# Kernel tuning notes

Measured on AMD Instinct MI355X. Metric: run time of the kernel, lower is better.

## Reference

```python
import jax, jax.numpy as jnp
import numpy as np

B, HH, WW, C = 2, 128, 128, 256
HEADS, KA, DR = 8, 3, 4
D = C // DR // HEADS          # 8 per-head channels
KK = KA * KA                  # 9 neighborhood positions
ATTN_DIM = KK * HEADS         # 72
DIMS = (ATTN_DIM // 4, ATTN_DIM // 2, ATTN_DIM)  # gnConv dims [18,36,72] (order=3)
SD = sum(DIMS)                # 126
S = 1.0                       # self.scale = s in __init__ (overrides qk scale)


def conv2d(x, w, b, pad, groups=1):
    out = jax.lax.conv_general_dilated(
        x, w, (1, 1), [(pad, pad), (pad, pad)],
        dimension_numbers=("NCHW", "OIHW", "NCHW"), feature_group_count=groups)
    return out + b[None, :, None, None]


def setup_inputs() -> dict:
    key = jax.random.key(0)
    ks = jax.random.split(key, 16)
    def rn(i, shape, s=0.02):
        return jax.random.normal(ks[i], shape, dtype=jnp.float32) * s
    return {
        "x": jax.random.normal(ks[0], (B, HH * WW, C), dtype=jnp.float32),
        "qkv_w": rn(1, (C, 3 * C // DR)),
        "qkv_b": jnp.zeros((3 * C // DR,), jnp.float32),
        "dc1_dw_w": rn(2, (D, 1, KA, KA)),
        "dc1_dw_b": jnp.zeros((D,), jnp.float32),
        "dc1_pw_w": rn(3, (KK * D, D, 3, 3)),
        "dc1_pw_b": jnp.zeros((KK * D,), jnp.float32),
        "dc2_dw_w": rn(4, (D, 1, KA, KA)),
        "dc2_dw_b": jnp.zeros((D,), jnp.float32),
        "dc2_pw_w": rn(5, (KK * D, D, 3, 3)),
        "dc2_pw_b": jnp.zeros((KK * D,), jnp.float32),
        "rpb": rn(6, (1, HEADS, 1, KK, 1, 1)),
        "pin_w": rn(7, (2 * ATTN_DIM, ATTN_DIM, 1, 1)),
        "pin_b": jnp.zeros((2 * ATTN_DIM,), jnp.float32),
        "dw7_w": rn(8, (SD, 1, 7, 7)),
        "dw7_b": jnp.zeros((SD,), jnp.float32),
        "dw5_w": rn(9, (SD, 1, 5, 5)),
        "dw5_b": jnp.zeros((SD,), jnp.float32),
        "dw3_w": rn(10, (SD, 1, 3, 3)),
        "dw3_b": jnp.zeros((SD,), jnp.float32),
        "pw1_w": rn(11, (DIMS[1], DIMS[0], 1, 1)),
        "pw1_b": jnp.zeros((DIMS[1],), jnp.float32),
        "pw2_w": rn(12, (DIMS[2], DIMS[1], 1, 1)),
        "pw2_b": jnp.zeros((DIMS[2],), jnp.float32),
        "pout_w": rn(13, (ATTN_DIM, ATTN_DIM, 1, 1)),
        "pout_b": jnp.zeros((ATTN_DIM,), jnp.float32),
        "proj_w": rn(14, (C // DR, C)),
        "proj_b": jnp.zeros((C,), jnp.float32),
        "H": HH,
        "W": WW,
    }


def reference(x, qkv_w, qkv_b, dc1_dw_w, dc1_dw_b, dc1_pw_w, dc1_pw_b,
              dc2_dw_w, dc2_dw_b, dc2_pw_w, dc2_pw_b, rpb, pin_w, pin_b,
              dw7_w, dw7_b, dw5_w, dw5_b, dw3_w, dw3_b,
              pw1_w, pw1_b, pw2_w, pw2_b, pout_w, pout_b, proj_w, proj_b, H, W):
    Bx, N, Cx = x.shape
    xi = x.reshape(Bx, H, W, Cx)
    qkv = xi @ qkv_w + qkv_b                                   # (B,H,W,3C/DR)
    f = jnp.transpose(qkv, (0, 3, 1, 2)).reshape(Bx * HEADS, 3 * D, H, W)
    q = (f[:, :D] * S).reshape(Bx, HEADS, D, 1, H, W)
    k_in = f[:, D:2 * D]                                       # (B*heads, D, H, W)
    v_in = f[:, 2 * D:]

    def dep(y):  # shared dep_conv + dep_conv1: KAxKA depthwise then 3x3 D->KK*D expand
        a = conv2d(conv2d(y, dc1_dw_w, dc1_dw_b, KA // 2, groups=D), dc1_pw_w, dc1_pw_b, 1)
        b2 = conv2d(conv2d(y, dc2_dw_w, dc2_dw_b, KA // 2, groups=D), dc2_pw_w, dc2_pw_b, 1)
        return (a + b2).reshape(Bx, HEADS, D, KK, H, W)

    k = dep(k_in) + rpb                                        # relative position bias
    v = dep(v_in)
    attn1 = jax.nn.softmax((q * k).sum(2, keepdims=True), axis=3)  # (B,heads,1,KK,H,W)

    # gnConv (recursive gated conv) on attention maps
    attn = attn1.reshape(Bx, HEADS * KK, H, W)                 # (B,72,H,W)
    fused = conv2d(attn, pin_w, pin_b, 0)                      # (B,144,H,W)
    pwa, abc = fused[:, :DIMS[0]], fused[:, DIMS[0]:]          # 18 / 126
    dw = conv2d(abc, dw7_w, dw7_b, 3, groups=SD)
    dw = conv2d(jax.nn.relu(dw), dw5_w, dw5_b, 2, groups=SD)
    dw = conv2d(jax.nn.relu(dw), dw3_w, dw3_b, 1, groups=SD) * S
    d0 = dw[:, :DIMS[0]]
    d1 = dw[:, DIMS[0]:DIMS[0] + DIMS[1]]
    d2 = dw[:, DIMS[0] + DIMS[1]:]
    g = pwa * d0
    g = conv2d(g, pw1_w, pw1_b, 0) * d1
    g = conv2d(g, pw2_w, pw2_b, 0) * d2
    g = conv2d(g, pout_w, pout_b, 0).reshape(Bx, HEADS, 1, KK, H, W)

    out = ((g * v) + (attn1 * v)).sum(3).reshape(Bx, Cx // DR, H, W)
    out = jnp.transpose(out, (0, 2, 3, 1)) @ proj_w + proj_b   # Linear C/DR -> C
    return out.reshape(Bx, N, Cx)
```

## Files before the change

kernel.cpp:

```cpp
#include <hip/hip_runtime.h>

#define IH 128
#define IW 128
#define NPI (IH*IW)

__global__ __launch_bounds__(256) void k_wt(const float* __restrict__ w1,
                                            const float* __restrict__ w2,
                                            const float* __restrict__ pin_w,
                                            const float* __restrict__ pw1_w,
                                            const float* __restrict__ pw2_w,
                                            const float* __restrict__ pout_w,
                                            float* __restrict__ wT,
                                            float* __restrict__ pinT,
                                            float* __restrict__ pw1T,
                                            float* __restrict__ pw2T,
                                            float* __restrict__ poutT) {
  int i = blockIdx.x * 256 + threadIdx.x;
  if (i < 5184) {
    int c = i / 72, dkk = i % 72;
    wT[dkk * 144 + c]      = w1[i];
    wT[dkk * 144 + 72 + c] = w2[i];
  } else if (i < 5184 + 10368) {
    int f = i - 5184;
    pinT[(f % 72) * 144 + f / 72] = pin_w[f];
  } else if (i < 5184 + 10368 + 648) {
    int f = i - 5184 - 10368;
    pw1T[(f % 18) * 36 + f / 18] = pw1_w[f];
  } else if (i < 5184 + 10368 + 648 + 2592) {
    int f = i - 5184 - 10368 - 648;
    pw2T[(f % 36) * 72 + f / 36] = pw2_w[f];
  } else if (i < 5184 + 10368 + 648 + 2592 + 5184) {
    int f = i - 5184 - 10368 - 648 - 2592;
    poutT[(f % 72) * 72 + f / 72] = pout_w[f];
  }
}

__global__ __launch_bounds__(256) void k_qkv(const float* __restrict__ x,
                                             const float* __restrict__ w,
                                             const float* __restrict__ bias,
                                             float* __restrict__ f) {
  __shared__ float xs[16][68];
  __shared__ float ws[16][196];
  int t = threadIdx.x;
  int p0 = blockIdx.x * 64;
  int b = p0 >> 14;
  int pp = p0 & (NPI - 1);
  int tx = t & 15, ty = t >> 4;
  int pxb = tx * 4;
  int jb = ty * 12;
  float acc[48];
#pragma unroll
  for (int jj = 0; jj < 12; ++jj) {
    float bv = bias[jb + jj];
#pragma unroll
    for (int px = 0; px < 4; ++px) acc[jj * 4 + px] = bv;
  }
  int spx = t >> 2;
  int sk = (t & 3) * 4;
#pragma unroll 1
  for (int c0 = 0; c0 < 256; c0 += 16) {
    float4 xv = *reinterpret_cast<const float4*>(x + (size_t)(p0 + spx) * 256 + c0 + sk);
    xs[sk + 0][spx] = xv.x;
    xs[sk + 1][spx] = xv.y;
    xs[sk + 2][spx] = xv.z;
    xs[sk + 3][spx] = xv.w;
#pragma unroll
    for (int r = 0; r < 3; ++r) {
      int flat = (r * 256 + t) * 4;
      int kk = flat / 192, jj = flat % 192;
      float4 wv = *reinterpret_cast<const float4*>(w + (size_t)(c0 + kk) * 192 + jj);
      *reinterpret_cast<float4*>(&ws[kk][jj]) = wv;
    }
    __syncthreads();
#pragma unroll 4
    for (int k = 0; k < 16; ++k) {
      float4 xr = *reinterpret_cast<const float4*>(&xs[k][pxb]);
      float4 w0 = *reinterpret_cast<const float4*>(&ws[k][jb]);
      float4 w1 = *reinterpret_cast<const float4*>(&ws[k][jb + 4]);
      float4 w2 = *reinterpret_cast<const float4*>(&ws[k][jb + 8]);
      const float xv4[4] = {xr.x, xr.y, xr.z, xr.w};
      const float wv12[12] = {w0.x, w0.y, w0.z, w0.w, w1.x, w1.y, w1.z, w1.w,
                              w2.x, w2.y, w2.z, w2.w};
#pragma unroll
      for (int jj = 0; jj < 12; ++jj)
#pragma unroll
        for (int px = 0; px < 4; ++px)
          acc[jj * 4 + px] = __builtin_fmaf(wv12[jj], xv4[px], acc[jj * 4 + px]);
    }
    __syncthreads();
  }
#pragma unroll
  for (int jj = 0; jj < 12; ++jj) {
    float4 o;
    o.x = acc[jj * 4 + 0]; o.y = acc[jj * 4 + 1];
    o.z = acc[jj * 4 + 2]; o.w = acc[jj * 4 + 3];
    *reinterpret_cast<float4*>(
        &f[((size_t)(b * 192 + jb + jj)) * NPI + pp + pxb]) = o;
  }
}

template <int MODE>
__global__ __launch_bounds__(256, 1) void k_dep(const float* __restrict__ f,
    const float* __restrict__ dwW1, const float* __restrict__ dwB1,
    const float* __restrict__ dwW2, const float* __restrict__ dwB2,
    const float* __restrict__ wT,  const float* __restrict__ pwB1,
    const float* __restrict__ pwB2, const float* __restrict__ rpb,
    const float* __restrict__ gout, const float* __restrict__ attn_in,
    float* __restrict__ outp) {
  __shared__ float kin[8][20][20];
  __shared__ float dwa[8][18][20];
  __shared__ float dwb[8][18][20];
  int t = threadIdx.x;
  int tile = blockIdx.x;
  int bh = blockIdx.y;
  int h = bh & 7;
  int y0 = (tile >> 3) << 4, x0 = (tile & 7) << 4;
  const float* src = f + ((size_t)(bh * 24 + (MODE ? 16 : 8))) * NPI;
  for (int idx = t; idx < 8 * 20 * 20; idx += 256) {
    int c = idx / 400, r = idx % 400, yy = r / 20, xx = r % 20;
    int ay = y0 - 2 + yy, ax = x0 - 2 + xx;
    float v = 0.f;
    if ((unsigned)ay < (unsigned)IH && (unsigned)ax < (unsigned)IW)
      v = src[c * NPI + ay * IW + ax];
    kin[c][yy][xx] = v;
  }
  __syncthreads();
  for (int idx = t; idx < 8 * 18 * 18; idx += 256) {
    int c = idx / 324, r = idx % 324, yy = r / 18, xx = r % 18;
    int ay = y0 - 1 + yy, ax = x0 - 1 + xx;
    float va = 0.f, vb = 0.f;
    if ((unsigned)ay < (unsigned)IH && (unsigned)ax < (unsigned)IW) {
      va = dwB1[c]; vb = dwB2[c];
#pragma unroll
      for (int ky = 0; ky < 3; ++ky)
#pragma unroll
        for (int kx = 0; kx < 3; ++kx) {
          float s = kin[c][yy + ky][xx + kx];
          va = __builtin_fmaf(dwW1[c * 9 + ky * 3 + kx], s, va);
          vb = __builtin_fmaf(dwW2[c * 9 + ky * 3 + kx], s, vb);
        }
    }
    dwa[c][yy][xx] = va;
    dwb[c][yy][xx] = vb;
  }
  __syncthreads();
  int ly = t >> 4, lx = t & 15;
  int p = (y0 + ly) * IW + (x0 + lx);
  float acc[72];
#pragma unroll
  for (int c = 0; c < 72; ++c) {
    acc[c] = pwB1[c] + pwB2[c];
    if (MODE == 0) acc[c] += rpb[h * 9 + (c % 9)];
  }
#pragma unroll 1
  for (int d = 0; d < 8; ++d) {
#pragma unroll
    for (int t9 = 0; t9 < 9; ++t9) {
      const int ky = t9 / 3, kx = t9 % 3;
      const float v1 = dwa[d][ly + ky][lx + kx];
      const float v2 = dwb[d][ly + ky][lx + kx];
      const float* wp = wT + (size_t)(d * 9 + t9) * 144;
#pragma unroll
      for (int c = 0; c < 72; ++c) {
        acc[c] = __builtin_fmaf(wp[c], v1, acc[c]);
        acc[c] = __builtin_fmaf(wp[72 + c], v2, acc[c]);
      }
    }
  }
  if (MODE == 0) {
    float q[8];
#pragma unroll
    for (int d = 0; d < 8; ++d) q[d] = f[((size_t)(bh * 24 + d)) * NPI + p];
    float e[9];
    float m = -1e30f;
#pragma unroll
    for (int kk = 0; kk < 9; ++kk) {
      float s = 0.f;
#pragma unroll
      for (int d = 0; d < 8; ++d) s = __builtin_fmaf(q[d], acc[d * 9 + kk], s);
      e[kk] = s;
      m = fmaxf(m, s);
    }
    float sum = 0.f;
#pragma unroll
    for (int kk = 0; kk < 9; ++kk) { e[kk] = __expf(e[kk] - m); sum += e[kk]; }
    float r = 1.f / sum;
#pragma unroll
    for (int kk = 0; kk < 9; ++kk)
      outp[((size_t)(bh * 9 + kk)) * NPI + p] = e[kk] * r;
  } else {
    float coef[9];
#pragma unroll
    for (int kk = 0; kk < 9; ++kk)
      coef[kk] = gout[((size_t)(bh * 9 + kk)) * NPI + p] +
                 attn_in[((size_t)(bh * 9 + kk)) * NPI + p];
#pragma unroll
    for (int d = 0; d < 8; ++d) {
      float s = 0.f;
#pragma unroll
      for (int kk = 0; kk < 9; ++kk) s = __builtin_fmaf(coef[kk], acc[d * 9 + kk], s);
      outp[((size_t)(bh * 8 + d)) * NPI + p] = s;
    }
  }
}

__global__ __launch_bounds__(256, 2) void k_pin(const float* __restrict__ attn,
                                                const float* __restrict__ pinT,
                                                const float* __restrict__ bias,
                                                float* __restrict__ fused) {
  int t = threadIdx.x, lane = t & 63;
  int wv = t >> 6;
  int gp = blockIdx.x * 64 + lane;
  int b = gp >> 14, p = gp & (NPI - 1);
  const float* ap = attn + (size_t)b * 72 * NPI + p;
  int jbase = wv * 36;
  float acc[36];
#pragma unroll
  for (int jj = 0; jj < 36; ++jj) acc[jj] = bias[jbase + jj];
#pragma unroll 2
  for (int i = 0; i < 72; ++i) {
    float ai = ap[(size_t)i * NPI];
    const float* wp = pinT + i * 144 + jbase;
#pragma unroll
    for (int jj = 0; jj < 36; ++jj)
      acc[jj] = __builtin_fmaf(wp[jj], ai, acc[jj]);
  }
#pragma unroll
  for (int jj = 0; jj < 36; ++jj)
    fused[((size_t)b * 144 + jbase + jj) * NPI + p] = acc[jj];
}

__global__ __launch_bounds__(256) void k_dwchain(const float* __restrict__ fused,
    const float* __restrict__ w7, const float* __restrict__ b7,
    const float* __restrict__ w5, const float* __restrict__ b5,
    const float* __restrict__ w3, const float* __restrict__ b3,
    float* __restrict__ dwout) {
  __shared__ float s_in[44][44];
  __shared__ float s_t7[38][38];
  __shared__ float s_t5[34][34];
  int t = threadIdx.x;
  int tile = blockIdx.x;
  int c = blockIdx.y;
  int b = blockIdx.z;
  int y0 = (tile >> 2) << 5, x0 = (tile & 3) << 5;
  const float* src = fused + ((size_t)b * 144 + 18 + c) * NPI;
  for (int idx = t; idx < 44 * 44; idx += 256) {
    int yy = idx / 44, xx = idx % 44;
    int ay = y0 - 6 + yy, ax = x0 - 6 + xx;
    s_in[yy][xx] = ((unsigned)ay < (unsigned)IH && (unsigned)ax < (unsigned)IW)
                       ? src[ay * IW + ax] : 0.f;
  }
  __syncthreads();
  for (int idx = t; idx < 38 * 38; idx += 256) {
    int yy = idx / 38, xx = idx % 38;
    int ay = y0 - 3 + yy, ax = x0 - 3 + xx;
    float s = 0.f;
    if ((unsigned)ay < (unsigned)IH && (unsigned)ax < (unsigned)IW) {
      s = b7[c];
#pragma unroll
      for (int ky = 0; ky < 7; ++ky)
#pragma unroll
        for (int kx = 0; kx < 7; ++kx)
          s = __builtin_fmaf(w7[c * 49 + ky * 7 + kx], s_in[yy + ky][xx + kx], s);
      s = fmaxf(s, 0.f);
    }
    s_t7[yy][xx] = s;
  }
  __syncthreads();
  for (int idx = t; idx < 34 * 34; idx += 256) {
    int yy = idx / 34, xx = idx % 34;
    int ay = y0 - 1 + yy, ax = x0 - 1 + xx;
    float s = 0.f;
    if ((unsigned)ay < (unsigned)IH && (unsigned)ax < (unsigned)IW) {
      s = b5[c];
#pragma unroll
      for (int ky = 0; ky < 5; ++ky)
#pragma unroll
        for (int kx = 0; kx < 5; ++kx)
          s = __builtin_fmaf(w5[c * 25 + ky * 5 + kx], s_t7[yy + ky][xx + kx], s);
      s = fmaxf(s, 0.f);
    }
    s_t5[yy][xx] = s;
  }
  __syncthreads();
  for (int idx = t; idx < 32 * 32; idx += 256) {
    int py = idx >> 5, px = idx & 31;
    float s = b3[c];
#pragma unroll
    for (int ky = 0; ky < 3; ++ky)
#pragma unroll
      for (int kx = 0; kx < 3; ++kx)
        s = __builtin_fmaf(w3[c * 9 + ky * 3 + kx], s_t5[py + ky][px + kx], s);
    dwout[((size_t)b * 126 + c) * NPI + (y0 + py) * IW + (x0 + px)] = s;
  }
}

__global__ __launch_bounds__(256, 2) void k_gchain(const float* __restrict__ fused,
    const float* __restrict__ dw,
    const float* __restrict__ pw1T, const float* __restrict__ pw1_b,
    const float* __restrict__ pw2T, const float* __restrict__ pw2_b,
    const float* __restrict__ poutT, const float* __restrict__ pout_b,
    float* __restrict__ gout) {
  __shared__ float t36[36][64];
  __shared__ float t72[72][64];
  int t = threadIdx.x, lane = t & 63;
  int wv = t >> 6;
  int gp = blockIdx.x * 64 + lane;
  int b = gp >> 14, p = gp & (NPI - 1);
  const float* fu = fused + (size_t)b * 144 * NPI + p;
  const float* dp = dw + (size_t)b * 126 * NPI + p;
  {
    int j0 = wv * 9;
    float acc[9];
#pragma unroll
    for (int j = 0; j < 9; ++j) acc[j] = pw1_b[j0 + j];
#pragma unroll
    for (int i = 0; i < 18; ++i) {
      float g1 = fu[(size_t)i * NPI] * dp[(size_t)i * NPI];
      const float* wp = pw1T + i * 36 + j0;
#pragma unroll
      for (int j = 0; j < 9; ++j) acc[j] = __builtin_fmaf(wp[j], g1, acc[j]);
    }
#pragma unroll
    for (int j = 0; j < 9; ++j)
      t36[j0 + j][lane] = acc[j] * dp[(size_t)(18 + j0 + j) * NPI];
  }
  __syncthreads();
  {
    int j0 = wv * 18;
    float acc[18];
#pragma unroll
    for (int j = 0; j < 18; ++j) acc[j] = pw2_b[j0 + j];
#pragma unroll 2
    for (int i = 0; i < 36; ++i) {
      float ai = t36[i][lane];
      const float* wp = pw2T + i * 72 + j0;
#pragma unroll
      for (int j = 0; j < 18; ++j) acc[j] = __builtin_fmaf(wp[j], ai, acc[j]);
    }
#pragma unroll
    for (int j = 0; j < 18; ++j)
      t72[j0 + j][lane] = acc[j] * dp[(size_t)(54 + j0 + j) * NPI];
  }
  __syncthreads();
  {
    int j0 = wv * 18;
    float acc[18];
#pragma unroll
    for (int j = 0; j < 18; ++j) acc[j] = pout_b[j0 + j];
#pragma unroll 2
    for (int i = 0; i < 72; ++i) {
      float ai = t72[i][lane];
      const float* wp = poutT + i * 72 + j0;
#pragma unroll
      for (int j = 0; j < 18; ++j) acc[j] = __builtin_fmaf(wp[j], ai, acc[j]);
    }
#pragma unroll
    for (int j = 0; j < 18; ++j)
      gout[((size_t)b * 72 + j0 + j) * NPI + p] = acc[j];
  }
}

__global__ __launch_bounds__(256, 2) void k_proj(const float* __restrict__ pre,
                                                 const float* __restrict__ w,
                                                 const float* __restrict__ bias,
                                                 float* __restrict__ out) {
  int t = threadIdx.x;
  int blk = blockIdx.x;
  int b = (blk * 16) >> 14;
  int p0 = (blk * 16) & (NPI - 1);
  const float* pp = pre + (size_t)b * 64 * NPI + p0;
  float acc[16];
  float bs = bias[t];
#pragma unroll
  for (int px = 0; px < 16; ++px) acc[px] = bs;
#pragma unroll 2
  for (int i = 0; i < 64; ++i) {
    float wv = w[i * 256 + t];
    const float* sp = pp + (size_t)i * NPI;
#pragma unroll
    for (int px = 0; px < 16; ++px)
      acc[px] = __builtin_fmaf(wv, sp[px], acc[px]);
  }
#pragma unroll
  for (int px = 0; px < 16; ++px)
    out[((size_t)(b * NPI + p0 + px)) * 256 + t] = acc[px];
}

extern "C" void kernel_launch(void* const* d_in, const int* in_sizes, int n_in,
                              void* d_out, int out_size, void* d_ws, size_t ws_size,
                              hipStream_t stream) {
  const float* x        = (const float*)d_in[0];
  const float* qkv_w    = (const float*)d_in[1];
  const float* qkv_b    = (const float*)d_in[2];
  const float* dc1_dw_w = (const float*)d_in[3];
  const float* dc1_dw_b = (const float*)d_in[4];
  const float* dc1_pw_w = (const float*)d_in[5];
  const float* dc1_pw_b = (const float*)d_in[6];
  const float* dc2_dw_w = (const float*)d_in[7];
  const float* dc2_dw_b = (const float*)d_in[8];
  const float* dc2_pw_w = (const float*)d_in[9];
  const float* dc2_pw_b = (const float*)d_in[10];
  const float* rpb      = (const float*)d_in[11];
  const float* pin_w    = (const float*)d_in[12];
  const float* pin_b    = (const float*)d_in[13];
  const float* dw7_w    = (const float*)d_in[14];
  const float* dw7_b    = (const float*)d_in[15];
  const float* dw5_w    = (const float*)d_in[16];
  const float* dw5_b    = (const float*)d_in[17];
  const float* dw3_w    = (const float*)d_in[18];
  const float* dw3_b    = (const float*)d_in[19];
  const float* pw1_w    = (const float*)d_in[20];
  const float* pw1_b    = (const float*)d_in[21];
  const float* pw2_w    = (const float*)d_in[22];
  const float* pw2_b    = (const float*)d_in[23];
  const float* pout_w   = (const float*)d_in[24];
  const float* pout_b   = (const float*)d_in[25];
  const float* proj_w   = (const float*)d_in[26];
  const float* proj_b   = (const float*)d_in[27];
  (void)in_sizes; (void)n_in; (void)out_size; (void)ws_size;

  float* fbuf = (float*)d_out;
  float* ws    = (float*)d_ws;
  float* wT    = ws;
  float* pinT  = wT + 10368;
  float* pw1T  = pinT + 10368;
  float* pw2T  = pw1T + 648;
  float* poutT = pw2T + 2592;
  float* attn1 = poutT + 5184;
  float* fused = attn1 + 2359296;
  float* dwout = fused + 4718592;
  float* goutb = dwout + 4128768;
  float* pre   = goutb + 2359296;

  hipLaunchKernelGGL(k_wt, dim3(94), dim3(256), 0, stream, dc1_pw_w, dc2_pw_w,
                     pin_w, pw1_w, pw2_w, pout_w, wT, pinT, pw1T, pw2T, poutT);
  hipLaunchKernelGGL(k_qkv, dim3(512), dim3(256), 0, stream, x, qkv_w, qkv_b, fbuf);
  hipLaunchKernelGGL((k_dep<0>), dim3(64, 16), dim3(256), 0, stream, fbuf,
                     dc1_dw_w, dc1_dw_b, dc2_dw_w, dc2_dw_b, wT, dc1_pw_b, dc2_pw_b,
                     rpb, (const float*)nullptr, (const float*)nullptr, attn1);
  hipLaunchKernelGGL(k_pin, dim3(512), dim3(256), 0, stream, attn1, pinT, pin_b, fused);
  hipLaunchKernelGGL(k_dwchain, dim3(16, 126, 2), dim3(256), 0, stream, fused,
                     dw7_w, dw7_b, dw5_w, dw5_b, dw3_w, dw3_b, dwout);
  hipLaunchKernelGGL(k_gchain, dim3(512), dim3(256), 0, stream, fused, dwout,
                     pw1T, pw1_b, pw2T, pw2_b, poutT, pout_b, goutb);
  hipLaunchKernelGGL((k_dep<1>), dim3(64, 16), dim3(256), 0, stream, fbuf,
                     dc1_dw_w, dc1_dw_b, dc2_dw_w, dc2_dw_b, wT, dc1_pw_b, dc2_pw_b,
                     rpb, goutb, attn1, pre);
  hipLaunchKernelGGL(k_proj, dim3(2048), dim3(256), 0, stream, pre, proj_w, proj_b,
                     (float*)d_out);
}
```

Baseline: 482.1 us.

## Split k_dep output accumulation into two halves to cut register pressure

The deformable-conv kernel now computes its 72 output channels in two passes of 36 accumulators each instead of holding all 72 at once. The softmax dot product and the value reduction are carried across the halves as partial sums, and the min-blocks launch bound of 1 is dropped. Fewer live registers should allow more waves per CU to hide LDS and global latency. The cost is that the 3x3 depthwise neighbourhood reads from shared memory are done twice.

```diff
diff --git a/kernel.cpp b/kernel.cpp
--- a/kernel.cpp
+++ b/kernel.cpp
@@ -100,7 +100,7 @@
 }
 
 template <int MODE>
-__global__ __launch_bounds__(256, 1) void k_dep(const float* __restrict__ f,
+__global__ __launch_bounds__(256) void k_dep(const float* __restrict__ f,
     const float* __restrict__ dwW1, const float* __restrict__ dwB1,
     const float* __restrict__ dwW2, const float* __restrict__ dwB2,
     const float* __restrict__ wT,  const float* __restrict__ pwB1,
@@ -146,60 +146,80 @@
   __syncthreads();
   int ly = t >> 4, lx = t & 15;
   int p = (y0 + ly) * IW + (x0 + lx);
-  float acc[72];
-#pragma unroll
-  for (int c = 0; c < 72; ++c) {
-    acc[c] = pwB1[c] + pwB2[c];
-    if (MODE == 0) acc[c] += rpb[h * 9 + (c % 9)];
-  }
-#pragma unroll 1
-  for (int d = 0; d < 8; ++d) {
-#pragma unroll
-    for (int t9 = 0; t9 < 9; ++t9) {
-      const int ky = t9 / 3, kx = t9 % 3;
-      const float v1 = dwa[d][ly + ky][lx + kx];
-      const float v2 = dwb[d][ly + ky][lx + kx];
-      const float* wp = wT + (size_t)(d * 9 + t9) * 144;
-#pragma unroll
-      for (int c = 0; c < 72; ++c) {
-        acc[c] = __builtin_fmaf(wp[c], v1, acc[c]);
-        acc[c] = __builtin_fmaf(wp[72 + c], v2, acc[c]);
-      }
-    }
-  }
+  float q[8]; float coef[9];
   if (MODE == 0) {
-    float q[8];
 #pragma unroll
     for (int d = 0; d < 8; ++d) q[d] = f[((size_t)(bh * 24 + d)) * NPI + p];
-    float e[9];
-    float m = -1e30f;
-#pragma unroll
-    for (int kk = 0; kk < 9; ++kk) {
-      float s = 0.f;
-#pragma unroll
-      for (int d = 0; d < 8; ++d) s = __builtin_fmaf(q[d], acc[d * 9 + kk], s);
-      e[kk] = s;
-      m = fmaxf(m, s);
-    }
-    float sum = 0.f;
-#pragma unroll
-    for (int kk = 0; kk < 9; ++kk) { e[kk] = __expf(e[kk] - m); sum += e[kk]; }
-    float r = 1.f / sum;
-#pragma unroll
-    for (int kk = 0; kk < 9; ++kk)
-      outp[((size_t)(bh * 9 + kk)) * NPI + p] = e[kk] * r;
   } else {
-    float coef[9];
 #pragma unroll
     for (int kk = 0; kk < 9; ++kk)
       coef[kk] = gout[((size_t)(bh * 9 + kk)) * NPI + p] +
                  attn_in[((size_t)(bh * 9 + kk)) * NPI + p];
-#pragma unroll
+  }
+  float part[9];
+#pragma unroll
+  for (int half = 0; half < 2; ++half) {
+    const int c0 = half * 36;
+    float acc[36];
+#pragma unroll
+    for (int c = 0; c < 36; ++c) {
+      acc[c] = pwB1[c0 + c] + pwB2[c0 + c];
+      if (MODE == 0) acc[c] += rpb[h * 9 + (c % 9)];
+    }
+#pragma unroll 1
     for (int d = 0; d < 8; ++d) {
-      float s = 0.f;
-#pragma unroll
-      for (int kk = 0; kk < 9; ++kk) s = __builtin_fmaf(coef[kk], acc[d * 9 + kk], s);
-      outp[((size_t)(bh * 8 + d)) * NPI + p] = s;
+#pragma unroll
+      for (int t9 = 0; t9 < 9; ++t9) {
+        const int ky = t9 / 3, kx = t9 % 3;
+        const float v1 = dwa[d][ly + ky][lx + kx];
+        const float v2 = dwb[d][ly + ky][lx + kx];
+        const float* wp = wT + (size_t)(d * 9 + t9) * 144 + c0;
+#pragma unroll
+        for (int c = 0; c < 36; ++c) {
+          acc[c] = __builtin_fmaf(wp[c], v1, acc[c]);
+          acc[c] = __builtin_fmaf(wp[72 + c], v2, acc[c]);
+        }
+      }
+    }
+    if (MODE == 0) {
+      if (half == 0) {
+#pragma unroll
+        for (int kk = 0; kk < 9; ++kk) {
+          float s = 0.f;
+#pragma unroll
+          for (int dd = 0; dd < 4; ++dd)
+            s = __builtin_fmaf(q[dd], acc[dd * 9 + kk], s);
+          part[kk] = s;
+        }
+      } else {
+        float e[9];
+        float m = -1e30f;
+#pragma unroll
+        for (int kk = 0; kk < 9; ++kk) {
+          float s = part[kk];
+#pragma unroll
+          for (int dd = 0; dd < 4; ++dd)
+            s = __builtin_fmaf(q[4 + dd], acc[dd * 9 + kk], s);
+          e[kk] = s;
+          m = fmaxf(m, s);
+        }
+        float sum = 0.f;
+#pragma unroll
+        for (int kk = 0; kk < 9; ++kk) { e[kk] = __expf(e[kk] - m); sum += e[kk]; }
+        float r = 1.f / sum;
+#pragma unroll
+        for (int kk = 0; kk < 9; ++kk)
+          outp[((size_t)(bh * 9 + kk)) * NPI + p] = e[kk] * r;
+      }
+    } else {
+#pragma unroll
+      for (int dd = 0; dd < 4; ++dd) {
+        float s = 0.f;
+#pragma unroll
+        for (int kk = 0; kk < 9; ++kk)
+          s = __builtin_fmaf(coef[kk], acc[dd * 9 + kk], s);
+        outp[((size_t)(bh * 8 + half * 4 + dd)) * NPI + p] = s;
+      }
     }
   }
 }
```

Result: slower. 493.5 us (+2.4%).
